# Kernel tuning notes

Measured on AMD Instinct MI355X. Metric: run time of the kernel, lower is better.

## Reference

```python
import jax, jax.numpy as jnp
import numpy as np

B, T, C, H = 2, 2048, 1024, 16
D = C // H  # head dim 64


def setup_inputs() -> dict:
    key = jax.random.key(0)
    k1, k2, k3, k4, k5 = jax.random.split(key, 5)
    s = 0.02
    return {
        "x": jax.random.normal(k1, (B, T, C), jnp.float32),
        "w_attn": jax.random.normal(k2, (C, 3 * C), jnp.float32) * s,
        "b_attn": jnp.zeros((3 * C,), jnp.float32),
        "w_proj": jax.random.normal(k3, (C, C), jnp.float32) * s,
        "b_proj": jnp.zeros((C,), jnp.float32),
    }


def reference(x, w_attn, b_attn, w_proj, b_proj):
    b, t, c = x.shape
    qkv = x @ w_attn + b_attn  # [B,T,3C]
    q, k, v = jnp.split(qkv, 3, axis=-1)
    # [B,T,C] -> [B,H,T,D]
    q = q.reshape(b, t, H, D).transpose(0, 2, 1, 3)
    k = k.reshape(b, t, H, D).transpose(0, 2, 1, 3)
    v = v.reshape(b, t, H, D).transpose(0, 2, 1, 3)
    scores = jnp.einsum("bhqd,bhkd->bhqk", q, k) * (1.0 / jnp.sqrt(jnp.float32(D)))
    causal = jnp.tril(jnp.ones((t, t), bool))
    scores = jnp.where(causal[None, None], scores, jnp.float32(-jnp.inf))
    attn = jax.nn.softmax(scores, axis=-1)
    out = jnp.einsum("bhqk,bhkd->bhqd", attn, v)  # [B,H,T,D]
    out = out.transpose(0, 2, 1, 3).reshape(b, t, c)
    return out @ w_proj + b_proj
```

## Files before the change

### kernel.cpp

```cpp
#include <hip/hip_runtime.h>
#include <hip/hip_bf16.h>

#define B_ 2
#define T_ 2048
#define C_ 1024
#define H_ 16
#define D_ 64
#define M1 4096
#define N1 3072
#define K_ 1024

typedef __attribute__((ext_vector_type(8))) __bf16 bf16x8;
typedef __attribute__((ext_vector_type(4))) float f32x4;
typedef __attribute__((ext_vector_type(8))) unsigned short ushort8_t;
typedef __attribute__((ext_vector_type(4))) unsigned short ushort4_t;
typedef __attribute__((ext_vector_type(2))) unsigned int uint2_t;

static __device__ __forceinline__ unsigned short f2bf(float f) {
    unsigned int u = __builtin_bit_cast(unsigned int, f);
    u += 0x7fffu + ((u >> 16) & 1u);
    return (unsigned short)(u >> 16);
}
static __device__ __forceinline__ unsigned short f2bf_hw(float f) {
    return __builtin_bit_cast(unsigned short, (__bf16)f);
}
static __device__ __forceinline__ unsigned int packbf(float lo, float hi) {
    return (unsigned int)f2bf_hw(lo) | ((unsigned int)f2bf_hw(hi) << 16);
}
static __device__ __forceinline__ bf16x8 bload(const unsigned short* p) {
    return __builtin_bit_cast(bf16x8, *(const ushort8_t*)p);
}

#if defined(__has_builtin)
#if __has_builtin(__builtin_amdgcn_exp2f)
#define HAVE_EXP2_BUILTIN 1
#endif
#endif
static __device__ __forceinline__ float fexp2(float x) {
#ifdef HAVE_EXP2_BUILTIN
    return __builtin_amdgcn_exp2f(x);
#else
    float r; asm("v_exp_f32 %0, %1" : "=v"(r) : "v"(x)); return r;
#endif
}

typedef __attribute__((address_space(1))) const unsigned int gu32;
typedef __attribute__((address_space(3))) unsigned int lu32;
static __device__ __forceinline__ void gld16(const void* g, void* l) {
    __builtin_amdgcn_global_load_lds((gu32*)g, (lu32*)l, 16, 0, 0);
}

#define VMCNT(n) asm volatile("s_waitcnt vmcnt(" #n ")" ::: "memory")
#define LGKM0    asm volatile("s_waitcnt lgkmcnt(0)" ::: "memory")

__global__ void cast_x_kernel(const float* __restrict__ in,
                              unsigned short* __restrict__ out, int n4) {
    int idx = blockIdx.x * blockDim.x + threadIdx.x;
    int stride = gridDim.x * blockDim.x;
    for (int i = idx; i < n4; i += stride) {
        float4 v = ((const float4*)in)[i];
        ushort4_t o;
        o.x = f2bf(v.x); o.y = f2bf(v.y); o.z = f2bf(v.z); o.w = f2bf(v.w);
        ((ushort4_t*)out)[i] = o;
    }
}

__global__ void transpose_cast_kernel(const float* __restrict__ in,
                                      unsigned short* __restrict__ out,
                                      int K, int N) {
    __shared__ float tile[32][33];
    int tx = threadIdx.x & 31;
    int ty = threadIdx.x >> 5;
    int n0 = blockIdx.x * 32;
    int k0 = blockIdx.y * 32;
#pragma unroll
    for (int rr = 0; rr < 32; rr += 8)
        tile[ty + rr][tx] = in[(size_t)(k0 + ty + rr) * N + n0 + tx];
    __syncthreads();
#pragma unroll
    for (int rr = 0; rr < 32; rr += 8)
        out[(size_t)(n0 + ty + rr) * K + k0 + tx] = f2bf(tile[tx][ty + rr]);
}


#define GEMM_PROLOGUE(BXE, BYE)                                                          \
    __shared__ unsigned short As[2][128 * 32];                                           \
    __shared__ unsigned short Bs[2][128 * 32];                                           \
    const int tid = threadIdx.x;                                                         \
    const int lane = tid & 63;                                                           \
    const int wave = tid >> 6;                                                           \
    const int g = lane >> 4, cl = lane & 15;                                             \
    const int wr = (wave >> 1) * 64, wc = (wave & 1) * 64;                               \
    const int row0 = (BXE) * 128;                                                        \
    const int col0 = (BYE) * 128;                                                        \
    const int srow = tid >> 2;                                                \
    const int sgran = tid & 3;                                                           \
    f32x4 acc[4][4];                                                                     \
    _Pragma("unroll") for (int m = 0; m < 4; ++m)                                        \
        _Pragma("unroll") for (int n = 0; n < 4; ++n)                                    \
            acc[m][n] = (f32x4){0.f, 0.f, 0.f, 0.f};                                     \
    auto stage = [&](int buf, int k0) {                                                  \
        _Pragma("unroll") for (int c = 0; c < 2; ++c) {                                  \
            int r = srow + c * 64;                                                       \
            int lg = sgran ^ ((r >> 1) & 3);                                             \
            gld16(A + (size_t)(row0 + r) * K_ + k0 + lg * 8,                             \
                  (char*)&As[buf][0] + c * 4096 + wave * 1024);                          \
            gld16(Bt + (size_t)(col0 + r) * K_ + k0 + lg * 8,                            \
                  (char*)&Bs[buf][0] + c * 4096 + wave * 1024);                          \
        }                                                                                \
    };                                                                                   \
    stage(0, 0);                                                                         \
    int buf = 0;                                                                         \
    for (int k0 = 0; k0 < K_; k0 += 32) {                                                \
        if (k0 + 32 < K_) { stage(buf ^ 1, k0 + 32); VMCNT(4); }                         \
        else              { VMCNT(0); }                                                  \
        __builtin_amdgcn_s_barrier();                                                    \
        bf16x8 af[4], bfv[4];                                                            \
        _Pragma("unroll") for (int m = 0; m < 4; ++m) {                                  \
            int ra = wr + m * 16 + cl;                                                   \
            af[m] = bload(&As[buf][ra * 32 + (g ^ ((ra >> 1) & 3)) * 8]);                \
        }                                                                                \
        _Pragma("unroll") for (int n = 0; n < 4; ++n) {                                  \
            int rb = wc + n * 16 + cl;                                                   \
            bfv[n] = bload(&Bs[buf][rb * 32 + (g ^ ((rb >> 1) & 3)) * 8]);               \
        }                                                                                \
        _Pragma("unroll") for (int m = 0; m < 4; ++m)                                    \
            _Pragma("unroll") for (int n = 0; n < 4; ++n)                                \
                acc[m][n] = __builtin_amdgcn_mfma_f32_16x16x32_bf16(                     \
                    af[m], bfv[n], acc[m][n], 0, 0, 0);                                  \
        LGKM0;                                                                           \
        __builtin_amdgcn_s_barrier();                                                    \
        buf ^= 1;                                                                        \
    }

__global__ __launch_bounds__(256)
void gemm_qkv_kernel(const unsigned short* __restrict__ A,
                     const unsigned short* __restrict__ Bt,
                     const float* __restrict__ bias,
                     unsigned short* __restrict__ Qo,
                     unsigned short* __restrict__ Ko,
                     unsigned short* __restrict__ Vt)
{
    const int lin = blockIdx.x + gridDim.x * blockIdx.y;
    const int xcd = lin & 7;
    const int idx = lin >> 3;
    const int bx = (xcd >> 1) * 8 + (idx & 7);
    const int by = (xcd & 1) * 12 + (idx >> 3);

    GEMM_PROLOGUE(bx, by)

    const float QSCALE = 0.125f * 1.44269504088896340736f;
#pragma unroll
    for (int m = 0; m < 4; ++m) {
        int i0 = row0 + wr + m * 16 + g * 4;
        int b = i0 >> 11, t0 = i0 & 2047;
#pragma unroll
        for (int n = 0; n < 4; ++n) {
            int j = col0 + wc + n * 16 + cl;
            int which = j >> 10;
            int c = j & 1023;
            int h = c >> 6, d = c & 63;
            float bv = bias[j];
            size_t bh = (size_t)(b * H_ + h);
            float v0 = acc[m][n][0] + bv;
            float v1 = acc[m][n][1] + bv;
            float v2 = acc[m][n][2] + bv;
            float v3 = acc[m][n][3] + bv;
            if (which == 2) {
                uint2_t w;
                w.x = packbf(v0, v1);
                w.y = packbf(v2, v3);
                *(uint2_t*)&Vt[(bh * D_ + d) * T_ + t0] = w;
            } else if (which == 0) {
                Qo[(bh * T_ + t0 + 0) * D_ + d] = f2bf_hw(v0 * QSCALE);
                Qo[(bh * T_ + t0 + 1) * D_ + d] = f2bf_hw(v1 * QSCALE);
                Qo[(bh * T_ + t0 + 2) * D_ + d] = f2bf_hw(v2 * QSCALE);
                Qo[(bh * T_ + t0 + 3) * D_ + d] = f2bf_hw(v3 * QSCALE);
            } else {
                Ko[(bh * T_ + t0 + 0) * D_ + d] = f2bf_hw(v0);
                Ko[(bh * T_ + t0 + 1) * D_ + d] = f2bf_hw(v1);
                Ko[(bh * T_ + t0 + 2) * D_ + d] = f2bf_hw(v2);
                Ko[(bh * T_ + t0 + 3) * D_ + d] = f2bf_hw(v3);
            }
        }
    }
}

__global__ __launch_bounds__(256)
void gemm_proj_kernel(const unsigned short* __restrict__ A,
                      const unsigned short* __restrict__ Bt,
                      const float* __restrict__ bias,
                      float* __restrict__ out)
{
    GEMM_PROLOGUE(blockIdx.x, blockIdx.y)

#pragma unroll
    for (int m = 0; m < 4; ++m) {
        int i0 = row0 + wr + m * 16 + g * 4;
#pragma unroll
        for (int n = 0; n < 4; ++n) {
            int j = col0 + wc + n * 16 + cl;
            float bv = bias[j];
#pragma unroll
            for (int r = 0; r < 4; ++r)
                out[(size_t)(i0 + r) * C_ + j] = acc[m][n][r] + bv;
        }
    }
}

__global__ __launch_bounds__(256)
void attn_kernel(const unsigned short* __restrict__ Q,
                 const unsigned short* __restrict__ Kb,
                 const unsigned short* __restrict__ Vh_,
                 unsigned short* __restrict__ AO)
{
    __shared__ unsigned short Klds[2][64 * 64];
    __shared__ unsigned short Vlds[2][64 * 64];
    __shared__ unsigned short Plds[4][16 * 64];
    const int lin = blockIdx.x;
    const int idx = lin >> 3;
    const int bh  = (lin & 7) + 8 * (idx & 3);
    const int qt  = 31 - (idx >> 2);
    const int b = bh >> 4, h = bh & 15;
    const int tid = threadIdx.x;
    const int lane = tid & 63;
    const int wave = tid >> 6;
    const int g = lane >> 4, cl = lane & 15;

    const unsigned short* Qh = Q + (size_t)bh * T_ * D_;
    const unsigned short* Kh = Kb + (size_t)bh * T_ * D_;
    const unsigned short* Vh = Vh_ + (size_t)bh * D_ * T_;

    const int srow = tid >> 3;
    const int sg   = tid & 7;
    const int pswz = (cl & 7) << 4;

    auto stage = [&](int bufi, int kb) {
#pragma unroll
        for (int c = 0; c < 2; ++c) {
            int r = srow + c * 32;
            int lg = sg ^ (r & 7);
            gld16(Kh + (size_t)(kb + r) * D_ + lg * 8,
                  (char*)&Klds[bufi][0] + c * 4096 + wave * 1024);
            gld16(Vh + (size_t)r * T_ + kb + lg * 8,
                  (char*)&Vlds[bufi][0] + c * 4096 + wave * 1024);
        }
    };

    const int q0 = qt * 64 + wave * 16;
    const int tq = q0 + cl;

    bf16x8 qf[2];
#pragma unroll
    for (int c2 = 0; c2 < 2; ++c2)
        qf[c2] = bload(Qh + (size_t)(q0 + cl) * D_ + c2 * 32 + g * 8);

    f32x4 oacc[4];
#pragma unroll
    for (int n = 0; n < 4; ++n) oacc[n] = (f32x4){0.f, 0.f, 0.f, 0.f};
    float m_run = -INFINITY;
    float l_part = 0.f;

    const int nk = qt + 1;
    stage(0, 0);
    int buf = 0;
    for (int kt = 0; kt < nk; ++kt) {
        if (kt + 1 < nk) { stage(buf ^ 1, (kt + 1) * 64); VMCNT(4); }
        else             { VMCNT(0); }
        __builtin_amdgcn_s_barrier();

        const int kb = kt * 64;
        f32x4 sc[4];
        __builtin_amdgcn_s_setprio(1);
#pragma unroll
        for (int n = 0; n < 4; ++n) {
            sc[n] = (f32x4){0.f, 0.f, 0.f, 0.f};
#pragma unroll
            for (int c2 = 0; c2 < 2; ++c2) {
                int pg = (c2 * 4 + g) ^ (cl & 7);
                bf16x8 kf = bload(&Klds[buf][(n * 16 + cl) * 64 + pg * 8]);
                sc[n] = __builtin_amdgcn_mfma_f32_16x16x32_bf16(kf, qf[c2], sc[n], 0, 0, 0);
            }
        }
        __builtin_amdgcn_s_setprio(0);
        if (kt == qt) {
#pragma unroll
            for (int n = 0; n < 4; ++n) {
                int k4 = kb + n * 16 + g * 4;
#pragma unroll
                for (int r = 0; r < 4; ++r)
                    if (k4 + r > tq) sc[n][r] = -INFINITY;
            }
        }
        float mx[4];
#pragma unroll
        for (int n = 0; n < 4; ++n)
            mx[n] = fmaxf(fmaxf(sc[n][0], sc[n][1]), fmaxf(sc[n][2], sc[n][3]));
        float lm = fmaxf(fmaxf(mx[0], mx[1]), fmaxf(mx[2], mx[3]));
        if (!__all(lm <= m_run + 8.f)) {
            float vmax = lm;
            vmax = fmaxf(vmax, __shfl_xor(vmax, 16, 64));
            vmax = fmaxf(vmax, __shfl_xor(vmax, 32, 64));
            float mn = fmaxf(m_run, vmax);
            float alpha = fexp2(m_run - mn);
            l_part *= alpha;
#pragma unroll
            for (int n = 0; n < 4; ++n)
#pragma unroll
                for (int r = 0; r < 4; ++r) oacc[n][r] *= alpha;
            m_run = mn;
        }
        float p[4][4], psub[4];
#pragma unroll
        for (int n = 0; n < 4; ++n) {
#pragma unroll
            for (int r = 0; r < 4; ++r) p[n][r] = fexp2(sc[n][r] - m_run);
            psub[n] = (p[n][0] + p[n][1]) + (p[n][2] + p[n][3]);
        }
        l_part += (psub[0] + psub[1]) + (psub[2] + psub[3]);
#pragma unroll
        for (int n = 0; n < 4; ++n) {
            uint2_t w;
            w.x = packbf(p[n][0], p[n][1]);
            w.y = packbf(p[n][2], p[n][3]);
            *(uint2_t*)((char*)&Plds[wave][0] + ((cl * 128 + n * 32 + g * 8) ^ pswz)) = w;
        }
        bf16x8 pf[2];
#pragma unroll
        for (int kk = 0; kk < 2; ++kk)
            pf[kk] = bload((const unsigned short*)
                ((char*)&Plds[wave][0] + ((cl * 128 + kk * 64 + g * 16) ^ pswz)));
        __builtin_amdgcn_s_setprio(1);
#pragma unroll
        for (int n = 0; n < 4; ++n) {
#pragma unroll
            for (int kk = 0; kk < 2; ++kk) {
                int pg = (kk * 4 + g) ^ (cl & 7);
                bf16x8 vfr = bload(&Vlds[buf][(n * 16 + cl) * 64 + pg * 8]);
                oacc[n] = __builtin_amdgcn_mfma_f32_16x16x32_bf16(vfr, pf[kk], oacc[n], 0, 0, 0);
            }
        }
        __builtin_amdgcn_s_setprio(0);
        LGKM0;
        __builtin_amdgcn_s_barrier();
        buf ^= 1;
    }
    float lt = l_part;
    lt += __shfl_xor(lt, 16, 64);
    lt += __shfl_xor(lt, 32, 64);
    float inv = 1.f / lt;
#pragma unroll
    for (int n = 0; n < 4; ++n) {
        uint2_t w;
        w.x = packbf(oacc[n][0] * inv, oacc[n][1] * inv);
        w.y = packbf(oacc[n][2] * inv, oacc[n][3] * inv);
        *(uint2_t*)&AO[((size_t)b * T_ + tq) * C_ + h * D_ + n * 16 + g * 4] = w;
    }
}

extern "C" void kernel_launch(void* const* d_in, const int* in_sizes, int n_in,
                              void* d_out, int out_size, void* d_ws, size_t ws_size,
                              hipStream_t stream) {
    (void)in_sizes; (void)n_in; (void)out_size; (void)ws_size;
    const float* x      = (const float*)d_in[0];
    const float* w_attn = (const float*)d_in[1];
    const float* b_attn = (const float*)d_in[2];
    const float* w_proj = (const float*)d_in[3];
    const float* b_proj = (const float*)d_in[4];
    float* out = (float*)d_out;

    char* ws = (char*)d_ws;
    unsigned short* Xb  = (unsigned short*)(ws);
    unsigned short* Wt1 = (unsigned short*)(ws + ((size_t)8  << 20));
    unsigned short* Wt2 = (unsigned short*)(ws + ((size_t)14 << 20));
    unsigned short* Qb  = (unsigned short*)(ws + ((size_t)16 << 20));
    unsigned short* Kb  = (unsigned short*)(ws + ((size_t)24 << 20));
    unsigned short* Vt  = (unsigned short*)(ws + ((size_t)32 << 20));
    unsigned short* AO  = Xb;

    cast_x_kernel<<<1024, 256, 0, stream>>>(x, Xb, (M1 * K_) / 4);
    transpose_cast_kernel<<<dim3(N1 / 32, K_ / 32), 256, 0, stream>>>(w_attn, Wt1, K_, N1);
    transpose_cast_kernel<<<dim3(C_ / 32, K_ / 32), 256, 0, stream>>>(w_proj, Wt2, K_, C_);
    gemm_qkv_kernel<<<dim3(M1 / 128, N1 / 128), 256, 0, stream>>>(Xb, Wt1, b_attn, Qb, Kb, Vt);
    attn_kernel<<<1024, 256, 0, stream>>>(Qb, Kb, Vt, AO);
    gemm_proj_kernel<<<dim3(M1 / 128, C_ / 128), 256, 0, stream>>>(AO, Wt2, b_proj, out);
}
```

Before: 120.1 us.

## Process two query tiles per attention block to reuse K/V loads

Each attention workgroup now handles 128 query rows: every wave keeps two 16-row query fragments, one at offset 0 and one at offset 64. Each K/V tile staged into LDS is then used by twice as many MFMAs, which halves the grid and the global K/V traffic per query row. The first query half skips its final, fully masked key tile. In exchange, register pressure rises (hence launch_bounds(256,2)), the P staging buffer doubles, and there are half as many workgroups with longer causal imbalance per block, which could hurt occupancy and load balance.

```diff
diff --git a/kernel.cpp b/kernel.cpp
--- a/kernel.cpp
+++ b/kernel.cpp
@@ -208,7 +208,7 @@
     }
 }
 
-__global__ __launch_bounds__(256)
+__global__ __launch_bounds__(256, 2)
 void attn_kernel(const unsigned short* __restrict__ Q,
                  const unsigned short* __restrict__ Kb,
                  const unsigned short* __restrict__ Vh_,
@@ -216,11 +216,11 @@
 {
     __shared__ unsigned short Klds[2][64 * 64];
     __shared__ unsigned short Vlds[2][64 * 64];
-    __shared__ unsigned short Plds[4][16 * 64];
+    __shared__ unsigned short Plds[4][32 * 64];
     const int lin = blockIdx.x;
     const int idx = lin >> 3;
     const int bh  = (lin & 7) + 8 * (idx & 3);
-    const int qt  = 31 - (idx >> 2);
+    const int qt  = 15 - (idx >> 2);
     const int b = bh >> 4, h = bh & 15;
     const int tid = threadIdx.x;
     const int lane = tid & 63;
@@ -247,21 +247,27 @@
         }
     };
 
-    const int q0 = qt * 64 + wave * 16;
-    const int tq = q0 + cl;
-
-    bf16x8 qf[2];
-#pragma unroll
-    for (int c2 = 0; c2 < 2; ++c2)
-        qf[c2] = bload(Qh + (size_t)(q0 + cl) * D_ + c2 * 32 + g * 8);
-
-    f32x4 oacc[4];
-#pragma unroll
-    for (int n = 0; n < 4; ++n) oacc[n] = (f32x4){0.f, 0.f, 0.f, 0.f};
-    float m_run = -INFINITY;
-    float l_part = 0.f;
-
-    const int nk = qt + 1;
+    const int q0 = qt * 128 + wave * 16;
+    int tq[2];
+    tq[0] = q0 + cl;
+    tq[1] = q0 + 64 + cl;
+
+    bf16x8 qf[2][2];
+#pragma unroll
+    for (int hq = 0; hq < 2; ++hq)
+#pragma unroll
+        for (int c2 = 0; c2 < 2; ++c2)
+            qf[hq][c2] = bload(Qh + (size_t)(q0 + hq * 64 + cl) * D_ + c2 * 32 + g * 8);
+
+    f32x4 oacc[2][4];
+#pragma unroll
+    for (int hq = 0; hq < 2; ++hq)
+#pragma unroll
+        for (int n = 0; n < 4; ++n) oacc[hq][n] = (f32x4){0.f, 0.f, 0.f, 0.f};
+    float m_run[2] = {-INFINITY, -INFINITY};
+    float l_part[2] = {0.f, 0.f};
+
+    const int nk = 2 * qt + 2;
     stage(0, 0);
     int buf = 0;
     for (int kt = 0; kt < nk; ++kt) {
@@ -270,66 +276,92 @@
         __builtin_amdgcn_s_barrier();
 
         const int kb = kt * 64;
-        f32x4 sc[4];
+        const bool do0 = (kt < nk - 1);
+        f32x4 sc[2][4];
+#pragma unroll
+        for (int hq = 0; hq < 2; ++hq)
+#pragma unroll
+            for (int n = 0; n < 4; ++n) sc[hq][n] = (f32x4){0.f, 0.f, 0.f, 0.f};
         __builtin_amdgcn_s_setprio(1);
 #pragma unroll
         for (int n = 0; n < 4; ++n) {
-            sc[n] = (f32x4){0.f, 0.f, 0.f, 0.f};
 #pragma unroll
             for (int c2 = 0; c2 < 2; ++c2) {
                 int pg = (c2 * 4 + g) ^ (cl & 7);
                 bf16x8 kf = bload(&Klds[buf][(n * 16 + cl) * 64 + pg * 8]);
-                sc[n] = __builtin_amdgcn_mfma_f32_16x16x32_bf16(kf, qf[c2], sc[n], 0, 0, 0);
+                if (do0)
+                    sc[0][n] = __builtin_amdgcn_mfma_f32_16x16x32_bf16(kf, qf[0][c2], sc[0][n], 0, 0, 0);
+                sc[1][n] = __builtin_amdgcn_mfma_f32_16x16x32_bf16(kf, qf[1][c2], sc[1][n], 0, 0, 0);
             }
         }
         __builtin_amdgcn_s_setprio(0);
-        if (kt == qt) {
+        if (kt == nk - 2) {
 #pragma unroll
             for (int n = 0; n < 4; ++n) {
                 int k4 = kb + n * 16 + g * 4;
 #pragma unroll
                 for (int r = 0; r < 4; ++r)
-                    if (k4 + r > tq) sc[n][r] = -INFINITY;
-            }
-        }
-        float mx[4];
-#pragma unroll
-        for (int n = 0; n < 4; ++n)
-            mx[n] = fmaxf(fmaxf(sc[n][0], sc[n][1]), fmaxf(sc[n][2], sc[n][3]));
-        float lm = fmaxf(fmaxf(mx[0], mx[1]), fmaxf(mx[2], mx[3]));
-        if (!__all(lm <= m_run + 8.f)) {
-            float vmax = lm;
-            vmax = fmaxf(vmax, __shfl_xor(vmax, 16, 64));
-            vmax = fmaxf(vmax, __shfl_xor(vmax, 32, 64));
-            float mn = fmaxf(m_run, vmax);
-            float alpha = fexp2(m_run - mn);
-            l_part *= alpha;
+                    if (k4 + r > tq[0]) sc[0][n][r] = -INFINITY;
+            }
+        }
+        if (kt == nk - 1) {
+#pragma unroll
+            for (int n = 0; n < 4; ++n) {
+                int k4 = kb + n * 16 + g * 4;
+#pragma unroll
+                for (int r = 0; r < 4; ++r)
+                    if (k4 + r > tq[1]) sc[1][n][r] = -INFINITY;
+            }
+        }
+        float p[2][4][4];
+#pragma unroll
+        for (int hq = 0; hq < 2; ++hq) {
+            if (hq == 0 && !do0) continue;
+            float mx[4];
 #pragma unroll
             for (int n = 0; n < 4; ++n)
-#pragma unroll
-                for (int r = 0; r < 4; ++r) oacc[n][r] *= alpha;
-            m_run = mn;
-        }
-        float p[4][4], psub[4];
-#pragma unroll
-        for (int n = 0; n < 4; ++n) {
-#pragma unroll
-            for (int r = 0; r < 4; ++r) p[n][r] = fexp2(sc[n][r] - m_run);
-            psub[n] = (p[n][0] + p[n][1]) + (p[n][2] + p[n][3]);
-        }
-        l_part += (psub[0] + psub[1]) + (psub[2] + psub[3]);
-#pragma unroll
-        for (int n = 0; n < 4; ++n) {
-            uint2_t w;
-            w.x = packbf(p[n][0], p[n][1]);
-            w.y = packbf(p[n][2], p[n][3]);
-            *(uint2_t*)((char*)&Plds[wave][0] + ((cl * 128 + n * 32 + g * 8) ^ pswz)) = w;
-        }
-        bf16x8 pf[2];
-#pragma unroll
-        for (int kk = 0; kk < 2; ++kk)
-            pf[kk] = bload((const unsigned short*)
-                ((char*)&Plds[wave][0] + ((cl * 128 + kk * 64 + g * 16) ^ pswz)));
+                mx[n] = fmaxf(fmaxf(sc[hq][n][0], sc[hq][n][1]),
+                              fmaxf(sc[hq][n][2], sc[hq][n][3]));
+            float lm = fmaxf(fmaxf(mx[0], mx[1]), fmaxf(mx[2], mx[3]));
+            if (!__all(lm <= m_run[hq] + 8.f)) {
+                float vmax = lm;
+                vmax = fmaxf(vmax, __shfl_xor(vmax, 16, 64));
+                vmax = fmaxf(vmax, __shfl_xor(vmax, 32, 64));
+                float mn = fmaxf(m_run[hq], vmax);
+                float alpha = fexp2(m_run[hq] - mn);
+                l_part[hq] *= alpha;
+#pragma unroll
+                for (int n = 0; n < 4; ++n)
+#pragma unroll
+                    for (int r = 0; r < 4; ++r) oacc[hq][n][r] *= alpha;
+                m_run[hq] = mn;
+            }
+            float psub[4];
+#pragma unroll
+            for (int n = 0; n < 4; ++n) {
+#pragma unroll
+                for (int r = 0; r < 4; ++r) p[hq][n][r] = fexp2(sc[hq][n][r] - m_run[hq]);
+                psub[n] = (p[hq][n][0] + p[hq][n][1]) + (p[hq][n][2] + p[hq][n][3]);
+            }
+            l_part[hq] += (psub[0] + psub[1]) + (psub[2] + psub[3]);
+#pragma unroll
+            for (int n = 0; n < 4; ++n) {
+                uint2_t w;
+                w.x = packbf(p[hq][n][0], p[hq][n][1]);
+                w.y = packbf(p[hq][n][2], p[hq][n][3]);
+                *(uint2_t*)((char*)&Plds[wave][0] +
+                    (((hq * 16 + cl) * 128 + n * 32 + g * 8) ^ pswz)) = w;
+            }
+        }
+        bf16x8 pf[2][2];
+#pragma unroll
+        for (int hq = 0; hq < 2; ++hq) {
+            if (hq == 0 && !do0) continue;
+#pragma unroll
+            for (int kk = 0; kk < 2; ++kk)
+                pf[hq][kk] = bload((const unsigned short*)((char*)&Plds[wave][0] +
+                    (((hq * 16 + cl) * 128 + kk * 64 + g * 16) ^ pswz)));
+        }
         __builtin_amdgcn_s_setprio(1);
 #pragma unroll
         for (int n = 0; n < 4; ++n) {
@@ -337,7 +369,9 @@
             for (int kk = 0; kk < 2; ++kk) {
                 int pg = (kk * 4 + g) ^ (cl & 7);
                 bf16x8 vfr = bload(&Vlds[buf][(n * 16 + cl) * 64 + pg * 8]);
-                oacc[n] = __builtin_amdgcn_mfma_f32_16x16x32_bf16(vfr, pf[kk], oacc[n], 0, 0, 0);
+                if (do0)
+                    oacc[0][n] = __builtin_amdgcn_mfma_f32_16x16x32_bf16(vfr, pf[0][kk], oacc[0][n], 0, 0, 0);
+                oacc[1][n] = __builtin_amdgcn_mfma_f32_16x16x32_bf16(vfr, pf[1][kk], oacc[1][n], 0, 0, 0);
             }
         }
         __builtin_amdgcn_s_setprio(0);
@@ -345,16 +379,19 @@
         __builtin_amdgcn_s_barrier();
         buf ^= 1;
     }
-    float lt = l_part;
-    lt += __shfl_xor(lt, 16, 64);
-    lt += __shfl_xor(lt, 32, 64);
-    float inv = 1.f / lt;
-#pragma unroll
-    for (int n = 0; n < 4; ++n) {
-        uint2_t w;
-        w.x = packbf(oacc[n][0] * inv, oacc[n][1] * inv);
-        w.y = packbf(oacc[n][2] * inv, oacc[n][3] * inv);
-        *(uint2_t*)&AO[((size_t)b * T_ + tq) * C_ + h * D_ + n * 16 + g * 4] = w;
+#pragma unroll
+    for (int hq = 0; hq < 2; ++hq) {
+        float lt = l_part[hq];
+        lt += __shfl_xor(lt, 16, 64);
+        lt += __shfl_xor(lt, 32, 64);
+        float inv = 1.f / lt;
+#pragma unroll
+        for (int n = 0; n < 4; ++n) {
+            uint2_t w;
+            w.x = packbf(oacc[hq][n][0] * inv, oacc[hq][n][1] * inv);
+            w.y = packbf(oacc[hq][n][2] * inv, oacc[hq][n][3] * inv);
+            *(uint2_t*)&AO[((size_t)b * T_ + tq[hq]) * C_ + h * D_ + n * 16 + g * 4] = w;
+        }
     }
 }
 
@@ -382,6 +419,6 @@
     transpose_cast_kernel<<<dim3(N1 / 32, K_ / 32), 256, 0, stream>>>(w_attn, Wt1, K_, N1);
     transpose_cast_kernel<<<dim3(C_ / 32, K_ / 32), 256, 0, stream>>>(w_proj, Wt2, K_, C_);
     gemm_qkv_kernel<<<dim3(M1 / 128, N1 / 128), 256, 0, stream>>>(Xb, Wt1, b_attn, Qb, Kb, Vt);
-    attn_kernel<<<1024, 256, 0, stream>>>(Qb, Kb, Vt, AO);
+    attn_kernel<<<512, 256, 0, stream>>>(Qb, Kb, Vt, AO);
     gemm_proj_kernel<<<dim3(M1 / 128, C_ / 128), 256, 0, stream>>>(AO, Wt2, b_proj, out);
 }
```

Result: slower. 132.8 us (+10.6%).
